# Optimization experiments

Measured on AMD Instinct MI355X. Metric: run time of the kernel, lower is better.

## Reference

```python
import jax, jax.numpy as jnp
import numpy as np
from itertools import permutations

NUM_LAYERS = 3
K = 5  # fixed node degree -> every Hungarian sub-problem is 5x5
# one-hot permutation tensor: P1H[p, r, c] = 1 iff permutation p assigns row r -> col c
PERMS = np.array(list(permutations(range(K))), dtype=np.int32)          # [120, K]
P1H = (PERMS[:, :, None] == np.arange(K)[None, None, :]).astype(np.float32)  # [120, K, K]


def _mlp(x, W1, b1, W2, b2):
    # 2-layer MLP with ReLU (repo's MLP(in, hid, out, 2))
    return jax.nn.relu(x @ W1 + b1) @ W2 + b2


def _sinkhorn(src, itera):
    s = jax.nn.softmax(src, axis=1)  # row-max subtraction is built in
    for i in range(itera):
        s = s / jnp.sum(s, axis=i % 2, keepdims=True)
    return jnp.nan_to_num(s)


def _masked_softmax(src):
    s1 = jnp.nan_to_num(jax.nn.softmax(src, axis=1))
    s2 = jnp.nan_to_num(jax.nn.softmax(src, axis=0))
    return (s1 + s2) * 0.5


def setup_inputs() -> dict:
    key = jax.random.key(0)
    ks = jax.random.split(key, 12)
    n1 = n2 = 1024
    hid = 64
    adj1 = jax.random.randint(ks[0], (n1, K), 0, n1)
    adj2 = jax.random.randint(ks[1], (n2, K), 0, n2)
    # adjacency matrices consistent with the neighbor lists
    G1 = jnp.zeros((n1, n1), jnp.float32).at[jnp.arange(n1)[:, None], adj1].set(1.0)
    G2 = jnp.zeros((n2, n2), jnp.float32).at[jnp.arange(n2)[:, None], adj2].set(1.0)
    s = 0.1
    return {
        'G1': G1, 'G2': G2, 'adj1': adj1, 'adj2': adj2,
        'ro_W1': jax.random.normal(ks[2], (NUM_LAYERS, 1, hid), jnp.float32) * s,
        'ro_b1': jax.random.normal(ks[3], (NUM_LAYERS, hid), jnp.float32) * s,
        'ro_W2': jax.random.normal(ks[4], (NUM_LAYERS, hid, 1), jnp.float32) * s,
        'ro_b2': jax.random.normal(ks[5], (NUM_LAYERS, 1), jnp.float32) * s,
        'fin_W1': jax.random.normal(ks[6], (1, hid), jnp.float32) * s,
        'fin_b1': jax.random.normal(ks[7], (hid,), jnp.float32) * s,
        'fin_W2': jax.random.normal(ks[8], (hid, 1), jnp.float32) * s,
        'fin_b2': jax.random.normal(ks[9], (1,), jnp.float32) * s,
    }


def reference(G1, G2, adj1, adj2, ro_W1, ro_b1, ro_W2, ro_b2, fin_W1, fin_b1, fin_W2, fin_b2):
    n1 = G1.shape[0]
    n2 = G2.shape[0]
    d1 = jnp.sum(G1, axis=1)
    d2 = jnp.sum(G2, axis=1)
    ttheta = jnp.mean(d1)
    # S[i, j, 0] = -|d1[i] - d2[j]|
    S = -jnp.abs(d1[:, None] - d2[None, :])[..., None]  # [n1, n2, 1]
    p1h = jnp.asarray(P1H)
    for li in range(NUM_LAYERS):
        Wn = _sinkhorn(_mlp(S / ttheta, ro_W1[li], ro_b1[li], ro_W2[li], ro_b2[li]).squeeze(-1), 5)
        W = jnp.log(Wn * (n1 * 1.5))
        W = jnp.where(jnp.isneginf(W), jnp.float32(-1e12), W)
        W = jnp.where(jnp.isposinf(W), jnp.float32(1e12), W)
        Wd = jax.lax.stop_gradient(W)  # matches W.detach().numpy()
        # small[a, b, r, c] = Wd[adj1[a, r], adj2[b, c]]  -> [n1, n2, K, K]
        small = jnp.transpose(Wd[adj1][:, :, adj2], (0, 2, 1, 3))
        # exact linear_sum_assignment(-small): maximize sum over the K! permutations
        scores = jnp.einsum('abrc,prc->abp', small, p1h)  # [n1, n2, 120]
        X1 = jnp.max(scores, axis=-1)                      # [n1, n2]
        S = X1[..., None]
    out = _masked_softmax(_mlp(S, fin_W1, fin_b1, fin_W2, fin_b2).squeeze(-1))
    return out
```

## Files before the change

### kernel.cpp

```cpp
#include <hip/hip_runtime.h>
#include <math.h>

#define N 1024
#define NB 256
#define KD 5
#define SL 8
#define NT 126
#define MAGIC 0x13572468
#define FSTRIDE 32
#define FREGION (NB * FSTRIDE + FSTRIDE)


__device__ __forceinline__ float load_sc(const float* p){
  return __hip_atomic_load(p, __ATOMIC_RELAXED, __HIP_MEMORY_SCOPE_AGENT);
}
__device__ __forceinline__ void store_sc(float* p, float v){
  __hip_atomic_store(p, v, __ATOMIC_RELAXED, __HIP_MEMORY_SCOPE_AGENT);
}
__device__ __forceinline__ int load_sci(const int* p){
  return __hip_atomic_load(p, __ATOMIC_RELAXED, __HIP_MEMORY_SCOPE_AGENT);
}
__device__ __forceinline__ void store_sci(int* p, int v){
  __hip_atomic_store(p, v, __ATOMIC_RELAXED, __HIP_MEMORY_SCOPE_AGENT);
}

__device__ __forceinline__ void gbarS(int* flg){
  __builtin_amdgcn_s_waitcnt(0);
  __syncthreads();
  const int t = threadIdx.x, B = blockIdx.x;
  int* go = flg + NB * FSTRIDE;
  if (B == 0){
    if (t > 0 && t < NB){
      while (load_sci(&flg[t * FSTRIDE]) != MAGIC) __builtin_amdgcn_s_sleep(1);
    }
    __syncthreads();
    if (t == 0) store_sci(go, MAGIC);
  } else {
    if (t == 0){
      store_sci(&flg[B * FSTRIDE], MAGIC);
      while (load_sci(go) != MAGIC) __builtin_amdgcn_s_sleep(1);
    }
    __syncthreads();
  }
}

__device__ __forceinline__ float wred_sum(float v){
#pragma unroll
  for (int off = 32; off > 0; off >>= 1) v += __shfl_down(v, off);
  return v;
}
__device__ __forceinline__ void bsum4(float v[4], float* s64){
  float w0 = wred_sum(v[0]), w1 = wred_sum(v[1]), w2 = wred_sum(v[2]), w3 = wred_sum(v[3]);
  __syncthreads();
  int wv = threadIdx.x >> 6;
  if ((threadIdx.x & 63) == 0){ s64[wv*4] = w0; s64[wv*4+1] = w1; s64[wv*4+2] = w2; s64[wv*4+3] = w3; }
  __syncthreads();
  float r0 = 0.f, r1 = 0.f, r2 = 0.f, r3 = 0.f;
#pragma unroll
  for (int i = 0; i < 16; ++i){ r0 += s64[i*4]; r1 += s64[i*4+1]; r2 += s64[i*4+2]; r3 += s64[i*4+3]; }
  v[0] = r0; v[1] = r1; v[2] = r2; v[3] = r3;
}

__device__ __forceinline__ int distinct5(const int* v){
  int c = 0;
#pragma unroll
  for (int r = 0; r < KD; ++r){
    bool dup = false;
#pragma unroll
    for (int s = 0; s < r; ++s) dup = dup || (v[s] == v[r]);
    c += dup ? 0 : 1;
  }
  return c;
}
__device__ __forceinline__ void sort5(int* s){
#pragma unroll
  for (int i = 0; i < 4; ++i)
#pragma unroll
    for (int j = 0; j < 4 - i; ++j){
      int a = s[j], b = s[j+1];
      s[j] = min(a, b); s[j+1] = max(a, b);
    }
}
__device__ __forceinline__ int msrank(const int* c5){
  const int C_[6][5] = { {0,0,0,0,0},
                         {1,1,1,1,1},
                         {1,2,3,4,5},
                         {1,3,6,10,15},
                         {1,4,10,20,35},
                         {1,5,15,35,70} };
  int rank = 0, prev = 0;
#pragma unroll
  for (int i = 0; i < 5; ++i){
    for (int v = prev; v < c5[i]; ++v) rank += C_[5 - v][4 - i];
    prev = c5[i];
  }
  return rank;
}

#define DP5(ACCESS, OUT) {                                        \
  float f[32]; f[0] = 0.f;                                        \
  _Pragma("unroll")                                               \
  for (int r = 0; r < KD; ++r){                                   \
    float tr[KD];                                                 \
    _Pragma("unroll")                                             \
    for (int c = 0; c < KD; ++c) tr[c] = (ACCESS);                \
    _Pragma("unroll")                                             \
    for (int m = 1; m < 32; ++m){                                 \
      if (__popc(m) == r + 1){                                    \
        float best = -3.0e38f;                                    \
        _Pragma("unroll")                                         \
        for (int c = 0; c < KD; ++c)                              \
          if (m & (1 << c)) best = fmaxf(best, f[m ^ (1 << c)] + tr[c]); \
        f[m] = best;                                              \
      }                                                           \
    }                                                             \
  }                                                               \
  OUT = f[31];                                                    \
}

__device__ __forceinline__ void pwl_build(int t,
    const float* __restrict__ w1g, const float* __restrict__ b1g,
    const float* __restrict__ w2g, const float* __restrict__ b2g,
    float* ux, float* udA, float* udB,
    float* xss, float* dAs, float* dBs,
    float* Atb, float* Btb, float* sA0B0)
{
  if (t < 64){
    float w1 = w1g[t], bb = b1g[t], w2v = w2g[t];
    float xk, sdA, sdB, a0t = 0.f, b0t = 0.f;
    if (w1 != 0.f){
      xk = -bb / w1;
      float dA = w1 * w2v, dB = bb * w2v;
      if (w1 > 0.f){ sdA = dA;  sdB = dB; }
      else         { sdA = -dA; sdB = -dB; a0t = dA; b0t = dB; }
    } else {
      xk = 3.0e38f; sdA = 0.f; sdB = 0.f;
      b0t = fmaxf(bb, 0.f) * w2v;
    }
    ux[t] = xk; udA[t] = sdA; udB[t] = sdB;
    float A0 = wred_sum(a0t);
    float B0 = wred_sum(b0t);
    if (t == 0){ sA0B0[0] = A0; sA0B0[1] = B0 + b2g[0]; }
  }
  __syncthreads();
  if (t < 64){
    float xk = ux[t]; int rank = 0;
    for (int j = 0; j < 64; ++j){
      float xj = ux[j];
      rank += (xj < xk || (xj == xk && j < t)) ? 1 : 0;
    }
    xss[rank] = ux[t]; dAs[rank] = udA[t]; dBs[rank] = udB[t];
  }
  __syncthreads();
  if (t < 65){
    float sa = sA0B0[0], sb = sA0B0[1];
    for (int r = 0; r < t; ++r){ sa += dAs[r]; sb += dBs[r]; }
    Atb[t] = sa; Btb[t] = sb;
  }
  __syncthreads();
}

__global__ __launch_bounds__(1024) void
kFused(const int* __restrict__ adj1, const int* __restrict__ adj2,
       const float* __restrict__ roW1, const float* __restrict__ roB1,
       const float* __restrict__ roW2, const float* __restrict__ roB2,
       const float* __restrict__ fW1, const float* __restrict__ fB1,
       const float* __restrict__ fW2, const float* __restrict__ fB2,
       float* __restrict__ tY1g,
       float* __restrict__ C1B, float* __restrict__ C2B, float* __restrict__ C3B,
       float* __restrict__ CFB, float* __restrict__ Rg,
       float* __restrict__ outp,
       int* __restrict__ flg)
{
  __shared__ __align__(16) char uS[20 * N * 4 + N * 4];
  float* tY1 = (float*)uS;
  float (*rows20)[N] = (float (*)[N])uS;
  float* lc = (float*)(uS + 20 * N * 4);
  __shared__ unsigned char t2c[NT][5];
  __shared__ unsigned char sg1[N], sg2[N];
  __shared__ unsigned short st1[N], st2[N];
  __shared__ int h1[8], h2[8];
  __shared__ int cnt1T[NT], cnt2T[NT];
  __shared__ float A1[NT], B1[NT];
  __shared__ float sY0[25], slR0[5], slC0[5], stt2[2];
  __shared__ float slR1[NT], slC1[NT];
  __shared__ float vq[NT], vC[NT], vqi[NT], vCi[NT];
  __shared__ float s64[64], sAv[4];
  __shared__ float ux[64], udA[64], udB[64], xss[64], dAs[64], dBs[64];
  __shared__ float Atb[65], Btb[65], sA0B0[2];
  __shared__ float xs3[64], A3t[65], B3t[65];

  const int t = threadIdx.x, B = blockIdx.x;
  const float L1536 = logf(1536.0f);

  if (t < 8){ h1[t] = 0; h2[t] = 0; }
  if (t < NT){ cnt1T[t] = 0; cnt2T[t] = 0; }
#pragma unroll 1
  for (int key = t; key < 3125; key += 1024){
    int d[5]; int k2 = key;
#pragma unroll
    for (int i = 0; i < 5; ++i){ d[i] = k2 % 5; k2 /= 5; }
    if (d[0] <= d[1] && d[1] <= d[2] && d[2] <= d[3] && d[3] <= d[4]){
      int r = msrank(d);
#pragma unroll
      for (int i = 0; i < 5; ++i) t2c[r][i] = (unsigned char)d[i];
    }
  }
  int a2[KD], a1v[KD];
#pragma unroll
  for (int c = 0; c < KD; ++c) a2[c] = adj2[t * KD + c];
#pragma unroll
  for (int r = 0; r < KD; ++r) a1v[r] = adj1[t * KD + r];
  {
    int c2 = distinct5(a2) - 1, c1 = distinct5(a1v) - 1;
    sg2[t] = (unsigned char)c2; sg1[t] = (unsigned char)c1;
    atomicAdd(&h2[c2], 1);
    atomicAdd(&h1[c1], 1);
  }
  __syncthreads();

  {
    int c5[KD];
#pragma unroll
    for (int r = 0; r < KD; ++r) c5[r] = sg1[a1v[r]];
    sort5(c5);
    int ty = msrank(c5);
    st1[t] = (unsigned short)ty; atomicAdd(&cnt1T[ty], 1);
  }
  {
    int c5[KD];
#pragma unroll
    for (int c = 0; c < KD; ++c) c5[c] = sg2[a2[c]];
    sort5(c5);
    int ty = msrank(c5);
    st2[t] = (unsigned short)ty; atomicAdd(&cnt2T[ty], 1);
  }

  if (t < 64){
    float cnt1[5], cnt2[5];
#pragma unroll
    for (int g = 0; g < 5; ++g){ cnt1[g] = (float)h1[g]; cnt2[g] = (float)h2[g]; }
    float tt = 0.f;
#pragma unroll
    for (int g = 0; g < 5; ++g) tt += (float)(g + 1) * cnt1[g];
    tt *= (1.0f / 1024.0f);
    float tab[5];
#pragma unroll 1
    for (int i = 0; i < 5; ++i){
      float x = -(float)i / tt;
      float acc = roB2[0];
      for (int k = 0; k < 64; ++k){
        float hh = fmaxf(fmaf(x, roW1[k], roB1[k]), 0.f);
        acc = fmaf(hh, roW2[k], acc);
      }
      tab[i] = acc;
    }
    float Ee[5][5];
#pragma unroll
    for (int g = 0; g < 5; ++g)
#pragma unroll
      for (int h = 0; h < 5; ++h) Ee[g][h] = expf(tab[abs(g - h)]);
    float q0[5], C1c[5], q1[5], C2c[5], q2[5], C3c[5];
#pragma unroll
    for (int g = 0; g < 5; ++g){
      float s = 0.f;
#pragma unroll
      for (int h = 0; h < 5; ++h) s += cnt2[h] * Ee[g][h];
      q0[g] = s;
    }
#pragma unroll
    for (int h = 0; h < 5; ++h){
      float s = 0.f;
#pragma unroll
      for (int g = 0; g < 5; ++g) s += cnt1[g] * Ee[g][h] / q0[g];
      C1c[h] = s;
    }
#pragma unroll
    for (int g = 0; g < 5; ++g){
      float s = 0.f;
#pragma unroll
      for (int h = 0; h < 5; ++h) s += cnt2[h] * Ee[g][h] / C1c[h];
      q1[g] = s;
    }
#pragma unroll
    for (int h = 0; h < 5; ++h){
      float s = 0.f;
#pragma unroll
      for (int g = 0; g < 5; ++g) s += cnt1[g] * Ee[g][h] / q1[g];
      C2c[h] = s;
    }
#pragma unroll
    for (int g = 0; g < 5; ++g){
      float s = 0.f;
#pragma unroll
      for (int h = 0; h < 5; ++h) s += cnt2[h] * Ee[g][h] / C2c[h];
      q2[g] = s;
    }
#pragma unroll
    for (int h = 0; h < 5; ++h){
      float s = 0.f;
#pragma unroll
      for (int g = 0; g < 5; ++g) s += cnt1[g] * Ee[g][h] / q2[g];
      C3c[h] = s;
    }
    if (t == 0){
#pragma unroll
      for (int g = 0; g < 5; ++g){
#pragma unroll
        for (int h = 0; h < 5; ++h) sY0[g * 5 + h] = tab[abs(g - h)];
        slR0[g] = -logf(q2[g]);
        slC0[g] = logf(C3c[g]);
      }
      stt2[0] = tt;
    }
  } else if (t < 128){
    int l = t - 64;
    const float* w1g = roW1 + 64;
    const float* b1g = roB1 + 64;
    const float* w2g = roW2 + 64;
    const float* b2g = roB2 + 1;
    float w1 = w1g[l], bb = b1g[l], w2v = w2g[l];
    float xk, sdA, sdB, a0t = 0.f, b0t = 0.f;
    if (w1 != 0.f){
      xk = -bb / w1;
      float dA = w1 * w2v, dB = bb * w2v;
      if (w1 > 0.f){ sdA = dA;  sdB = dB; }
      else         { sdA = -dA; sdB = -dB; a0t = dA; b0t = dB; }
    } else {
      xk = 3.0e38f; sdA = 0.f; sdB = 0.f;
      b0t = fmaxf(bb, 0.f) * w2v;
    }
    ux[l] = xk; udA[l] = sdA; udB[l] = sdB;
    float A0 = wred_sum(a0t);
    float B0 = wred_sum(b0t);
    if (l == 0){ sA0B0[0] = A0; sA0B0[1] = B0 + b2g[0]; }
  }
  __syncthreads();

  if (t < 64){
    float xk = ux[t]; int rank = 0;
    for (int j = 0; j < 64; ++j){
      float xj = ux[j];
      rank += (xj < xk || (xj == xk && j < t)) ? 1 : 0;
    }
    xss[rank] = ux[t]; dAs[rank] = udA[t]; dBs[rank] = udB[t];
  } else if (t >= 256 && t < 256 + NT){
    int ty = t - 256;
    float sa = 5.0f * L1536, sb = 0.f;
#pragma unroll
    for (int i = 0; i < KD; ++i){
      int cl = t2c[ty][i];
      sa += slR0[cl];
      sb -= slC0[cl];
    }
    A1[ty] = sa; B1[ty] = sb;
  }
  __syncthreads();
  if (t < 65){
    float sa = sA0B0[0], sb = sA0B0[1];
    for (int r = 0; r < t; ++r){ sa += dAs[r]; sb += dBs[r]; }
    Atb[t] = sa; Btb[t] = sb;
  }
  __syncthreads();

  const float tt = stt2[0];
  if (t < 63){
    int e = B + 256 * t;
    if (e < NT * NT){
      int tau = e / NT, ups = e - tau * NT;
      const unsigned char* G = t2c[tau];
      const unsigned char* H = t2c[ups];
      float D;
      DP5(sY0[(int)G[r] * 5 + (int)H[c]], D);
      float x = (A1[tau] + B1[ups] + D) / tt;
      int seg = 0;
#pragma unroll
      for (int s = 64; s; s >>= 1)
        if (seg + s <= 64 && xss[seg + s - 1] <= x) seg += s;
      store_sc(&tY1g[e], fmaf(Atb[seg], x, Btb[seg]));
    }
  }

  pwl_build(t, fW1, fB1, fW2, fB2,
            ux, udA, udB, xs3, dAs, dBs, A3t, B3t, sA0B0);

  gbarS(flg + 0 * FREGION);

  {
    float rv[16];
#pragma unroll
    for (int i = 0; i < 16; ++i){
      int e = t + 1024 * i;
      if (e < NT * NT) rv[i] = load_sc(&tY1g[e]);
    }
#pragma unroll
    for (int i = 0; i < 16; ++i){
      int e = t + 1024 * i;
      if (e < NT * NT) tY1[e] = rv[i];
    }
  }

  pwl_build(t, roW1 + 128, roB1 + 128, roW2 + 128, roB2 + 2,
            ux, udA, udB, xss, dAs, dBs, Atb, Btb, sA0B0);

  {
    int g = t >> 3, j = t & 7;
    float Er[16], Ec[16];
    if (g < NT){
#pragma unroll
      for (int i = 0; i < 16; ++i){
        int u = j + 8 * i;
        if (u < NT){
          Er[i] = (float)cnt2T[u] * expf(tY1[g * NT + u]);
          Ec[i] = (float)cnt1T[u] * expf(tY1[u * NT + g]);
        } else { Er[i] = 0.f; Ec[i] = 0.f; }
      }
    }
    if (g < NT){
      float acc = 0.f;
#pragma unroll
      for (int i = 0; i < 16; ++i){ int u = j + 8 * i; if (u < NT) acc += Er[i]; }
      acc += __shfl_down(acc, 4, 8); acc += __shfl_down(acc, 2, 8); acc += __shfl_down(acc, 1, 8);
      if (j == 0){ vq[g] = acc; vqi[g] = 1.0f / acc; }
    }
    __syncthreads();
    if (g < NT){
      float acc = 0.f;
#pragma unroll
      for (int i = 0; i < 16; ++i){ int u = j + 8 * i; if (u < NT) acc += Ec[i] * vqi[u]; }
      acc += __shfl_down(acc, 4, 8); acc += __shfl_down(acc, 2, 8); acc += __shfl_down(acc, 1, 8);
      if (j == 0){ vC[g] = acc; vCi[g] = 1.0f / acc; }
    }
    __syncthreads();
    if (g < NT){
      float acc = 0.f;
#pragma unroll
      for (int i = 0; i < 16; ++i){ int u = j + 8 * i; if (u < NT) acc += Er[i] * vCi[u]; }
      acc += __shfl_down(acc, 4, 8); acc += __shfl_down(acc, 2, 8); acc += __shfl_down(acc, 1, 8);
      if (j == 0){ vq[g] = acc; vqi[g] = 1.0f / acc; }
    }
    __syncthreads();
    if (g < NT){
      float acc = 0.f;
#pragma unroll
      for (int i = 0; i < 16; ++i){ int u = j + 8 * i; if (u < NT) acc += Ec[i] * vqi[u]; }
      acc += __shfl_down(acc, 4, 8); acc += __shfl_down(acc, 2, 8); acc += __shfl_down(acc, 1, 8);
      if (j == 0){ vC[g] = acc; vCi[g] = 1.0f / acc; }
    }
    __syncthreads();
    if (g < NT){
      float acc = 0.f;
#pragma unroll
      for (int i = 0; i < 16; ++i){ int u = j + 8 * i; if (u < NT) acc += Er[i] * vCi[u]; }
      acc += __shfl_down(acc, 4, 8); acc += __shfl_down(acc, 2, 8); acc += __shfl_down(acc, 1, 8);
      if (j == 0){ vq[g] = acc; vqi[g] = 1.0f / acc; }
    }
    __syncthreads();
    if (g < NT){
      float acc = 0.f;
#pragma unroll
      for (int i = 0; i < 16; ++i){ int u = j + 8 * i; if (u < NT) acc += Ec[i] * vqi[u]; }
      acc += __shfl_down(acc, 4, 8); acc += __shfl_down(acc, 2, 8); acc += __shfl_down(acc, 1, 8);
      if (j == 0) vC[g] = acc;
    }
    __syncthreads();
  }
  if (t < NT){ slR1[t] = -logf(vq[t]); slC1[t] = logf(vC[t]); }
  __syncthreads();

  if (t < 4){
    int a = 4 * B + t;
    float s = 5.0f * L1536;
#pragma unroll
    for (int r = 0; r < KD; ++r) s += slR1[st1[adj1[a * KD + r]]];
    sAv[t] = s;
  }
  int stc[KD];
  float Bv2 = 0.f;
#pragma unroll
  for (int c = 0; c < KD; ++c){ stc[c] = st2[a2[c]]; Bv2 -= slC1[stc[c]]; }
  __syncthreads();

  float y2[4];
#pragma unroll 1
  for (int rr = 0; rr < 4; ++rr){
    int str_[KD];
#pragma unroll
    for (int r = 0; r < KD; ++r) str_[r] = st1[adj1[(4 * B + rr) * KD + r]];
    float D;
    DP5(tY1[str_[r] * NT + stc[c]], D);
    float x = (sAv[rr] + Bv2 + D) / tt;
    int seg = 0;
#pragma unroll
    for (int s = 64; s; s >>= 1)
      if (seg + s <= 64 && xss[seg + s - 1] <= x) seg += s;
    y2[rr] = fmaf(Atb[seg], x, Btb[seg]);
  }
  float E[4], q4[4];
#pragma unroll
  for (int r = 0; r < 4; ++r){ E[r] = expf(y2[r]); q4[r] = E[r]; }
  bsum4(q4, s64);
  {
    float cp = 0.f;
#pragma unroll
    for (int r = 0; r < 4; ++r){
      store_sc(&outp[(size_t)(4 * B + r) * N + t], y2[r]);
      cp += E[r] / q4[r];
    }
    atomicAdd(&C1B[(size_t)(B & (SL - 1)) * N + t], cp);
  }

  gbarS(flg + 1 * FREGION);

  float rv20[20];
#pragma unroll
  for (int k = 0; k < 20; ++k){
    int src = adj1[(4 * B + (k / 5)) * KD + (k % 5)];
    rv20[k] = load_sc(&outp[(size_t)src * N + t]);
  }

  {
    float C = 0.f;
#pragma unroll
    for (int k = 0; k < SL; ++k) C += load_sc(&C1B[(size_t)k * N + t]);
    float iC = 1.0f / C;
#pragma unroll
    for (int r = 0; r < 4; ++r) q4[r] = E[r] * iC;
    bsum4(q4, s64);
    float cp = 0.f;
#pragma unroll
    for (int r = 0; r < 4; ++r) cp += E[r] / q4[r];
    atomicAdd(&C2B[(size_t)(B & (SL - 1)) * N + t], cp);
  }

#pragma unroll
  for (int k = 0; k < 20; ++k) rows20[k][t] = rv20[k];

  gbarS(flg + 2 * FREGION);
  {
    float C = 0.f;
#pragma unroll
    for (int k = 0; k < SL; ++k) C += load_sc(&C2B[(size_t)k * N + t]);
    float iC = 1.0f / C;
#pragma unroll
    for (int r = 0; r < 4; ++r) q4[r] = E[r] * iC;
    bsum4(q4, s64);
    float cp = 0.f;
#pragma unroll
    for (int r = 0; r < 4; ++r) cp += E[r] / q4[r];
    if (t < 4) store_sc(&Rg[4 * B + t], 1.0f / q4[t]);
    atomicAdd(&C3B[(size_t)(B & (SL - 1)) * N + t], cp);
  }

  gbarS(flg + 3 * FREGION);
  {
    float C = 0.f;
#pragma unroll
    for (int k = 0; k < SL; ++k) C += load_sc(&C3B[(size_t)k * N + t]);
    lc[t] = logf(C);
  }
  if (t >= 64 && t < 68){
    int a = 4 * B + (t - 64);
    float s = 5.0f * logf(1536.0f);
#pragma unroll
    for (int r = 0; r < KD; ++r) s += logf(load_sc(&Rg[adj1[a * KD + r]]));
    sAv[t - 64] = s;
  }
  __syncthreads();

  float Bvl = 0.f;
#pragma unroll
  for (int c = 0; c < KD; ++c) Bvl -= lc[a2[c]];

  float y[4];
#pragma unroll 1
  for (int rr = 0; rr < 4; ++rr){
    float D;
    DP5(rows20[rr * 5 + r][a2[c]], D);
    float x = sAv[rr] + Bvl + D;
    int seg = 0;
#pragma unroll
    for (int s = 64; s; s >>= 1)
      if (seg + s <= 64 && xs3[seg + s - 1] <= x) seg += s;
    y[rr] = fmaf(A3t[seg], x, B3t[seg]);
  }

  float e4[4];
#pragma unroll
  for (int r = 0; r < 4; ++r){ e4[r] = expf(y[r]); q4[r] = e4[r]; }
  bsum4(q4, s64);

  {
    float cp = 0.f;
#pragma unroll
    for (int r = 0; r < 4; ++r) cp += e4[r];
    atomicAdd(&CFB[(size_t)(B & (SL - 1)) * N + t], cp);
  }

  gbarS(flg + 4 * FREGION);
  float CF = 0.f;
#pragma unroll
  for (int k = 0; k < SL; ++k) CF += load_sc(&CFB[(size_t)k * N + t]);
  float iCF = 1.0f / CF;
#pragma unroll
  for (int r = 0; r < 4; ++r){
    float v = 0.5f * e4[r] * (1.0f / q4[r] + iCF);
    outp[(size_t)(4 * B + r) * N + t] = v;
  }
}

extern "C" void kernel_launch(void* const* d_in, const int* in_sizes, int n_in,
                              void* d_out, int out_size, void* d_ws, size_t ws_size,
                              hipStream_t stream){
  (void)in_sizes; (void)n_in; (void)out_size; (void)ws_size;
  const int*   adj1 = (const int*)d_in[2];
  const int*   adj2 = (const int*)d_in[3];
  const float* roW1 = (const float*)d_in[4];
  const float* roB1 = (const float*)d_in[5];
  const float* roW2 = (const float*)d_in[6];
  const float* roB2 = (const float*)d_in[7];
  const float* fW1  = (const float*)d_in[8];
  const float* fB1  = (const float*)d_in[9];
  const float* fW2  = (const float*)d_in[10];
  const float* fB2  = (const float*)d_in[11];
  float* out = (float*)d_out;

  float* Pp   = (float*)d_ws;
  float* Rg   = Pp + (size_t)4 * SL * N;
  float* tY1g = Rg + N;
  int*   flg  = (int*)(tY1g + NT * NT);

  kFused<<<NB, 1024, 0, stream>>>(adj1, adj2, roW1, roB1, roW2, roB2,
                                  fW1, fB1, fW2, fB2,
                                  tY1g,
                                  Pp + (size_t)0 * SL * N, Pp + (size_t)1 * SL * N,
                                  Pp + (size_t)2 * SL * N, Pp + (size_t)3 * SL * N,
                                  Rg, out, flg);
}
```

Before: 150.4 us.

## Hoist 5x5 assignment DPs before grid barriers and precompute exp table

Moves the layer-2 and layer-3 assignment DP computations so they run before the sinkhorn reductions and grid barriers that they do not depend on. This shortens the critical path after each barrier. The shared tY1 table is overwritten with exp values once, so the row and column sums no longer recompute expf per element. The DP max initialisation also changes to seed from the first candidate. This adds extra __syncthreads and keeps more values live in registers.

```diff
diff --git a/kernel.cpp b/kernel.cpp
--- a/kernel.cpp
+++ b/kernel.cpp
@@ -107,11 +107,15 @@
     _Pragma("unroll")                                             \
     for (int m = 1; m < 32; ++m){                                 \
       if (__popc(m) == r + 1){                                    \
-        float best = -3.0e38f;                                    \
+        float dpb = 0.f; bool dpi = true;                         \
         _Pragma("unroll")                                         \
         for (int c = 0; c < KD; ++c)                              \
-          if (m & (1 << c)) best = fmaxf(best, f[m ^ (1 << c)] + tr[c]); \
-        f[m] = best;                                              \
+          if (m & (1 << c)){                                      \
+            float dpv = f[m ^ (1 << c)] + tr[c];                  \
+            dpb = dpi ? dpv : fmaxf(dpb, dpv);                    \
+            dpi = false;                                          \
+          }                                                       \
+        f[m] = dpb;                                               \
       }                                                           \
     }                                                             \
   }                                                               \
@@ -386,22 +390,41 @@
 
   gbarS(flg + 0 * FREGION);
 
-  {
-    float rv[16];
-#pragma unroll
-    for (int i = 0; i < 16; ++i){
-      int e = t + 1024 * i;
-      if (e < NT * NT) rv[i] = load_sc(&tY1g[e]);
-    }
-#pragma unroll
-    for (int i = 0; i < 16; ++i){
-      int e = t + 1024 * i;
-      if (e < NT * NT) tY1[e] = rv[i];
-    }
+  float rv[16];
+#pragma unroll
+  for (int i = 0; i < 16; ++i){
+    int e = t + 1024 * i;
+    if (e < NT * NT) rv[i] = load_sc(&tY1g[e]);
+  }
+#pragma unroll
+  for (int i = 0; i < 16; ++i){
+    int e = t + 1024 * i;
+    if (e < NT * NT) tY1[e] = rv[i];
   }
 
   pwl_build(t, roW1 + 128, roB1 + 128, roW2 + 128, roB2 + 2,
             ux, udA, udB, xss, dAs, dBs, Atb, Btb, sA0B0);
+
+  int stc[KD];
+#pragma unroll
+  for (int c = 0; c < KD; ++c) stc[c] = st2[a2[c]];
+  float D2[4];
+#pragma unroll 1
+  for (int rr = 0; rr < 4; ++rr){
+    int str_[KD];
+#pragma unroll
+    for (int r = 0; r < KD; ++r) str_[r] = st1[adj1[(4 * B + rr) * KD + r]];
+    float D;
+    DP5(tY1[str_[r] * NT + stc[c]], D);
+    D2[rr] = D;
+  }
+  __syncthreads();
+#pragma unroll
+  for (int i = 0; i < 16; ++i){
+    int e = t + 1024 * i;
+    if (e < NT * NT) tY1[e] = expf(rv[i]);
+  }
+  __syncthreads();
 
   {
     int g = t >> 3, j = t & 7;
@@ -411,8 +434,8 @@
       for (int i = 0; i < 16; ++i){
         int u = j + 8 * i;
         if (u < NT){
-          Er[i] = (float)cnt2T[u] * expf(tY1[g * NT + u]);
-          Ec[i] = (float)cnt1T[u] * expf(tY1[u * NT + g]);
+          Er[i] = (float)cnt2T[u] * tY1[g * NT + u];
+          Ec[i] = (float)cnt1T[u] * tY1[u * NT + g];
         } else { Er[i] = 0.f; Ec[i] = 0.f; }
       }
     }
@@ -475,21 +498,15 @@
     for (int r = 0; r < KD; ++r) s += slR1[st1[adj1[a * KD + r]]];
     sAv[t] = s;
   }
-  int stc[KD];
   float Bv2 = 0.f;
 #pragma unroll
-  for (int c = 0; c < KD; ++c){ stc[c] = st2[a2[c]]; Bv2 -= slC1[stc[c]]; }
+  for (int c = 0; c < KD; ++c) Bv2 -= slC1[stc[c]];
   __syncthreads();
 
   float y2[4];
-#pragma unroll 1
+#pragma unroll
   for (int rr = 0; rr < 4; ++rr){
-    int str_[KD];
-#pragma unroll
-    for (int r = 0; r < KD; ++r) str_[r] = st1[adj1[(4 * B + rr) * KD + r]];
-    float D;
-    DP5(tY1[str_[r] * NT + stc[c]], D);
-    float x = (sAv[rr] + Bv2 + D) / tt;
+    float x = (sAv[rr] + Bv2 + D2[rr]) / tt;
     int seg = 0;
 #pragma unroll
     for (int s = 64; s; s >>= 1)
@@ -535,49 +552,55 @@
 
 #pragma unroll
   for (int k = 0; k < 20; ++k) rows20[k][t] = rv20[k];
-
-  gbarS(flg + 2 * FREGION);
-  {
-    float C = 0.f;
-#pragma unroll
-    for (int k = 0; k < SL; ++k) C += load_sc(&C2B[(size_t)k * N + t]);
-    float iC = 1.0f / C;
-#pragma unroll
-    for (int r = 0; r < 4; ++r) q4[r] = E[r] * iC;
-    bsum4(q4, s64);
-    float cp = 0.f;
-#pragma unroll
-    for (int r = 0; r < 4; ++r) cp += E[r] / q4[r];
-    if (t < 4) store_sc(&Rg[4 * B + t], 1.0f / q4[t]);
-    atomicAdd(&C3B[(size_t)(B & (SL - 1)) * N + t], cp);
-  }
-
-  gbarS(flg + 3 * FREGION);
-  {
-    float C = 0.f;
-#pragma unroll
-    for (int k = 0; k < SL; ++k) C += load_sc(&C3B[(size_t)k * N + t]);
-    lc[t] = logf(C);
-  }
-  if (t >= 64 && t < 68){
-    int a = 4 * B + (t - 64);
-    float s = 5.0f * logf(1536.0f);
-#pragma unroll
-    for (int r = 0; r < KD; ++r) s += logf(load_sc(&Rg[adj1[a * KD + r]]));
-    sAv[t - 64] = s;
-  }
-  __syncthreads();
-
-  float Bvl = 0.f;
-#pragma unroll
-  for (int c = 0; c < KD; ++c) Bvl -= lc[a2[c]];
-
-  float y[4];
+  __syncthreads();
+  float D3[4];
 #pragma unroll 1
   for (int rr = 0; rr < 4; ++rr){
     float D;
     DP5(rows20[rr * 5 + r][a2[c]], D);
-    float x = sAv[rr] + Bvl + D;
+    D3[rr] = D;
+  }
+
+  gbarS(flg + 2 * FREGION);
+  {
+    float C = 0.f;
+#pragma unroll
+    for (int k = 0; k < SL; ++k) C += load_sc(&C2B[(size_t)k * N + t]);
+    float iC = 1.0f / C;
+#pragma unroll
+    for (int r = 0; r < 4; ++r) q4[r] = E[r] * iC;
+    bsum4(q4, s64);
+    float cp = 0.f;
+#pragma unroll
+    for (int r = 0; r < 4; ++r) cp += E[r] / q4[r];
+    if (t < 4) store_sc(&Rg[4 * B + t], 1.0f / q4[t]);
+    atomicAdd(&C3B[(size_t)(B & (SL - 1)) * N + t], cp);
+  }
+
+  gbarS(flg + 3 * FREGION);
+  {
+    float C = 0.f;
+#pragma unroll
+    for (int k = 0; k < SL; ++k) C += load_sc(&C3B[(size_t)k * N + t]);
+    lc[t] = logf(C);
+  }
+  if (t >= 64 && t < 68){
+    int a = 4 * B + (t - 64);
+    float s = 5.0f * logf(1536.0f);
+#pragma unroll
+    for (int r = 0; r < KD; ++r) s += logf(load_sc(&Rg[adj1[a * KD + r]]));
+    sAv[t - 64] = s;
+  }
+  __syncthreads();
+
+  float Bvl = 0.f;
+#pragma unroll
+  for (int c = 0; c < KD; ++c) Bvl -= lc[a2[c]];
+
+  float y[4];
+#pragma unroll
+  for (int rr = 0; rr < 4; ++rr){
+    float x = sAv[rr] + Bvl + D3[rr];
     int seg = 0;
 #pragma unroll
     for (int s = 64; s; s >>= 1)
```

Result: no change. 150.3 us (-0.0%).
